# Kernel optimization log

Hardware: AMD Instinct MI355X
Metric: run time of the kernel (lower is better)

The kernel has to match this reference:

```python
import jax, jax.numpy as jnp
import numpy as np

NUM_USERS = 100000
NUM_ITEMS = 50000
N_NODES = NUM_USERS + NUM_ITEMS
LATENT_DIM = 64
N_LAYERS = 3
NNZ = 2400000
BATCH = 16384


def setup_inputs() -> dict:
    key = jax.random.key(0)
    k1, k2, k3, k4, k5, k6, k7 = jax.random.split(key, 7)
    user_emb = jax.random.normal(k1, (NUM_USERS, LATENT_DIM), dtype=jnp.float32) * 0.1
    item_emb = jax.random.normal(k2, (NUM_ITEMS, LATENT_DIM), dtype=jnp.float32) * 0.1
    edge_rows = jax.random.randint(k3, (NNZ,), 0, N_NODES, dtype=jnp.int32)
    edge_cols = jax.random.randint(k4, (NNZ,), 0, N_NODES, dtype=jnp.int32)
    # normalized-adjacency-like positive weights
    edge_vals = jax.random.uniform(k5, (NNZ,), dtype=jnp.float32) * 0.05
    user_input = jax.random.randint(k6, (BATCH,), 0, NUM_USERS, dtype=jnp.int64)
    item_input = jax.random.randint(k7, (BATCH,), 0, NUM_ITEMS, dtype=jnp.int64)
    return {
        "user_emb": user_emb,
        "item_emb": item_emb,
        "edge_rows": edge_rows,
        "edge_cols": edge_cols,
        "edge_vals": edge_vals,
        "user_input": user_input,
        "item_input": item_input,
    }


def _spmm(edge_rows, edge_cols, edge_vals, x):
    # sparse [N,N] @ dense [N,D] via gather + weighted segment-sum
    gathered = x[edge_cols] * edge_vals[:, None]  # [nnz, D]
    return jax.ops.segment_sum(gathered, edge_rows, num_segments=N_NODES)


def reference(user_emb, item_emb, edge_rows, edge_cols, edge_vals, user_input, item_input):
    all_emb = jnp.concatenate([user_emb, item_emb], axis=0)  # [N, D]
    acc = all_emb
    for _ in range(N_LAYERS):
        all_emb = _spmm(edge_rows, edge_cols, edge_vals, all_emb)
        acc = acc + all_emb
    light_out = acc / (N_LAYERS + 1)  # mean over stacked layer embeddings
    users_avg = light_out[:NUM_USERS]
    items_avg = light_out[NUM_USERS:]
    u = users_avg[user_input]  # [B, D]
    i = items_avg[item_input]  # [B, D]
    preds = jnp.sum(u * i, axis=1)  # [B]
    return preds
```

## Files before the change

kernel.cpp:

```cpp
#include <hip/hip_runtime.h>

#define NUM_USERS 100000
#define NUM_ITEMS 50000
#define N_NODES   150000
#define DIM       64
#define BATCH_N   16384
#define NPART     586

__global__ __launch_bounds__(256) void lg_init(const float4* __restrict__ user_emb,
                        const float4* __restrict__ item_emb,
                        float4* __restrict__ x,
                        float4* __restrict__ acc) {
    const long user4 = (long)NUM_USERS * DIM / 4;
    const long tot4  = (long)N_NODES  * DIM / 4;
    for (long i = blockIdx.x * (long)blockDim.x + threadIdx.x;
         i < tot4;
         i += (long)gridDim.x * blockDim.x) {
        float4 v = (i < user4) ? user_emb[i] : item_emb[i - user4];
        x[i]   = v;
        acc[i] = v;
    }
}

__global__ __launch_bounds__(256) void lg_hist(const int* __restrict__ rows,
                                               int* __restrict__ cnt, int nnz) {
    int e = blockIdx.x * blockDim.x + threadIdx.x;
    if (e < nnz) atomicAdd(&cnt[rows[e]], 1);
}

__global__ __launch_bounds__(256) void lg_scan1(const int* __restrict__ cnt,
                                                int* __restrict__ ptr,
                                                int* __restrict__ part) {
    __shared__ int s[256];
    int i = blockIdx.x * 256 + threadIdx.x;
    int v = (i < N_NODES) ? cnt[i] : 0;
    s[threadIdx.x] = v;
    __syncthreads();
    #pragma unroll
    for (int off = 1; off < 256; off <<= 1) {
        int t = (threadIdx.x >= off) ? s[threadIdx.x - off] : 0;
        __syncthreads();
        s[threadIdx.x] += t;
        __syncthreads();
    }
    if (i < N_NODES) ptr[i] = s[threadIdx.x] - v;
    if (threadIdx.x == 255) part[blockIdx.x] = s[255];
}

__global__ __launch_bounds__(64) void lg_scan2(int* __restrict__ part, int n) {
    int lane = threadIdx.x & 63;
    int run = 0;
    for (int base = 0; base < n; base += 64) {
        int i = base + lane;
        int v = (i < n) ? part[i] : 0;
        int orig = v;
        #pragma unroll
        for (int off = 1; off < 64; off <<= 1) {
            int t = __shfl_up(v, off, 64);
            if (lane >= off) v += t;
        }
        if (i < n) part[i] = run + v - orig;
        run += __shfl(v, 63, 64);
    }
}

__global__ __launch_bounds__(256) void lg_scan3(int* __restrict__ ptr,
                                                const int* __restrict__ part,
                                                int* __restrict__ cur) {
    int i = blockIdx.x * 256 + threadIdx.x;
    if (i < N_NODES) {
        int p = ptr[i] + part[blockIdx.x];
        ptr[i] = p;
        cur[i] = p;
    }
}

__global__ __launch_bounds__(256) void lg_scatter(const int* __restrict__ rows,
                           const int* __restrict__ cols,
                           const float* __restrict__ vals, int* __restrict__ cur,
                           int2* __restrict__ edges, int nnz) {
    int e = blockIdx.x * blockDim.x + threadIdx.x;
    if (e >= nnz) return;
    int r = rows[e];
    int pos = atomicAdd(&cur[r], 1);
    edges[pos] = make_int2(cols[e], __float_as_int(vals[e]));
}

template <bool WRITE_Y>
__global__ __launch_bounds__(256) void lg_spmm_csr(const int* __restrict__ ptr,
                            const int* __restrict__ cnt,
                            const int2* __restrict__ edges,
                            const float* __restrict__ x, float* __restrict__ y,
                            float* __restrict__ acc) {
    int r    = blockIdx.x * (blockDim.x >> 6) + (threadIdx.x >> 6);
    int lane = threadIdx.x & 63;
    if (r >= N_NODES) return;
    int start = __builtin_amdgcn_readfirstlane(ptr[r]);
    int len   = __builtin_amdgcn_readfirstlane(cnt[r]);
    const int2* __restrict__ ep = edges + start;
    float s0 = 0.0f, s1 = 0.0f;
    int j = 0;
    for (; j + 2 <= len; j += 2) {
        int2 e0 = ep[j];
        int2 e1 = ep[j + 1];
        s0 += __int_as_float(e0.y) * x[(long)e0.x * DIM + lane];
        s1 += __int_as_float(e1.y) * x[(long)e1.x * DIM + lane];
    }
    if (j < len) {
        int2 e0 = ep[j];
        s0 += __int_as_float(e0.y) * x[(long)e0.x * DIM + lane];
    }
    float sum = s0 + s1;
    long o = (long)r * DIM + lane;
    if (WRITE_Y) y[o] = sum;
    acc[o] += sum;
}

__global__ __launch_bounds__(256) void lg_dot(const float* __restrict__ acc,
                       const int*   __restrict__ uidx,
                       const int*   __restrict__ iidx,
                       float*       __restrict__ out,
                       int batch) {
    int b    = blockIdx.x * (blockDim.x >> 6) + (threadIdx.x >> 6);
    int lane = threadIdx.x & 63;
    if (b >= batch) return;
    long u = (long)uidx[b];
    long t = (long)NUM_USERS + iidx[b];
    float p = acc[u * DIM + lane] * acc[t * DIM + lane] * (1.0f / 16.0f);
    #pragma unroll
    for (int off = 32; off > 0; off >>= 1)
        p += __shfl_down(p, off, 64);
    if (lane == 0) out[b] = p;
}

extern "C" void kernel_launch(void* const* d_in, const int* in_sizes, int n_in,
                              void* d_out, int out_size, void* d_ws, size_t ws_size,
                              hipStream_t stream) {
    const float* user_emb  = (const float*)d_in[0];
    const float* item_emb  = (const float*)d_in[1];
    const int*   edge_rows = (const int*)  d_in[2];
    const int*   edge_cols = (const int*)  d_in[3];
    const float* edge_vals = (const float*)d_in[4];
    const int*   user_inp  = (const int*)  d_in[5];
    const int*   item_inp  = (const int*)  d_in[6];
    float*       out       = (float*)d_out;

    const int nnz = in_sizes[2];

    const size_t embBytes = (size_t)N_NODES * DIM * sizeof(float);
    const size_t nodeInts = (size_t)N_NODES * sizeof(int);
    const size_t need = 3 * embBytes + (size_t)nnz * 8 + 3 * nodeInts
                      + (size_t)NPART * sizeof(int);
    if (ws_size < need) return;

    char* ws = (char*)d_ws;
    float* x     = (float*)(ws);
    float* y     = (float*)(ws + embBytes);
    float* acc   = (float*)(ws + 2 * embBytes);
    int2*  edges = (int2*) (ws + 3 * embBytes);
    int*   cnt   = (int*)  (ws + 3 * embBytes + (size_t)nnz * 8);
    int*   ptr   = (int*)  (ws + 3 * embBytes + (size_t)nnz * 8 + nodeInts);
    int*   cur   = (int*)  (ws + 3 * embBytes + (size_t)nnz * 8 + 2 * nodeInts);
    int*   part  = (int*)  (ws + 3 * embBytes + (size_t)nnz * 8 + 3 * nodeInts);

    lg_init<<<2048, 256, 0, stream>>>((const float4*)user_emb,
                                      (const float4*)item_emb,
                                      (float4*)x, (float4*)acc);

    hipMemsetAsync(cnt, 0, nodeInts, stream);
    const int eb = (nnz + 255) / 256;
    lg_hist   <<<eb,    256, 0, stream>>>(edge_rows, cnt, nnz);
    lg_scan1  <<<NPART, 256, 0, stream>>>(cnt, ptr, part);
    lg_scan2  <<<1,      64, 0, stream>>>(part, NPART);
    lg_scan3  <<<NPART, 256, 0, stream>>>(ptr, part, cur);
    lg_scatter<<<eb,    256, 0, stream>>>(edge_rows, edge_cols, edge_vals,
                                          cur, edges, nnz);

    const int rowBlocks = (N_NODES + 3) / 4;
    lg_spmm_csr<true ><<<rowBlocks, 256, 0, stream>>>(ptr, cnt, edges, x, y, acc);
    lg_spmm_csr<true ><<<rowBlocks, 256, 0, stream>>>(ptr, cnt, edges, y, x, acc);
    lg_spmm_csr<false><<<rowBlocks, 256, 0, stream>>>(ptr, cnt, edges, x, y, acc);

    lg_dot<<<(BATCH_N + 3) / 4, 256, 0, stream>>>(acc, user_inp, item_inp,
                                                  out, BATCH_N);
}
```

Before: 703.9 us.

## Split edge scatter into row-range passes and unroll SpMM gather by four

The CSR scatter now runs as eight launches, each handling only edges whose destination row falls in one slice of the node range. This keeps the atomic cursor and edge-array write targets within a smaller footprint per pass, aiming for better cache locality of the random writes. The cost is re-reading the row array eight times. The SpMM inner loop is unrolled from two to four independent accumulators, and 64-bit index math is replaced by 32-bit shifts in SpMM and the dot kernel.

New measurement: 666.3 us. -5.3%, faster.

```diff
diff --git a/kernel.cpp b/kernel.cpp
--- a/kernel.cpp
+++ b/kernel.cpp
@@ -6,6 +6,8 @@
 #define DIM       64
 #define BATCH_N   16384
 #define NPART     586
+#define SC_PASSES 8
+#define SC_SLICE  18750
 
 __global__ __launch_bounds__(256) void lg_init(const float4* __restrict__ user_emb,
                         const float4* __restrict__ item_emb,
@@ -75,13 +77,14 @@
     }
 }
 
-__global__ __launch_bounds__(256) void lg_scatter(const int* __restrict__ rows,
+__global__ __launch_bounds__(256) void lg_scatter_pass(const int* __restrict__ rows,
                            const int* __restrict__ cols,
                            const float* __restrict__ vals, int* __restrict__ cur,
-                           int2* __restrict__ edges, int nnz) {
+                           int2* __restrict__ edges, int nnz, int lo, int hi) {
     int e = blockIdx.x * blockDim.x + threadIdx.x;
     if (e >= nnz) return;
     int r = rows[e];
+    if (r < lo || r >= hi) return;
     int pos = atomicAdd(&cur[r], 1);
     edges[pos] = make_int2(cols[e], __float_as_int(vals[e]));
 }
@@ -98,20 +101,24 @@
     int start = __builtin_amdgcn_readfirstlane(ptr[r]);
     int len   = __builtin_amdgcn_readfirstlane(cnt[r]);
     const int2* __restrict__ ep = edges + start;
-    float s0 = 0.0f, s1 = 0.0f;
+    float s0 = 0.0f, s1 = 0.0f, s2 = 0.0f, s3 = 0.0f;
     int j = 0;
-    for (; j + 2 <= len; j += 2) {
+    for (; j + 4 <= len; j += 4) {
         int2 e0 = ep[j];
         int2 e1 = ep[j + 1];
-        s0 += __int_as_float(e0.y) * x[(long)e0.x * DIM + lane];
-        s1 += __int_as_float(e1.y) * x[(long)e1.x * DIM + lane];
+        int2 e2 = ep[j + 2];
+        int2 e3 = ep[j + 3];
+        s0 += __int_as_float(e0.y) * x[(e0.x << 6) + lane];
+        s1 += __int_as_float(e1.y) * x[(e1.x << 6) + lane];
+        s2 += __int_as_float(e2.y) * x[(e2.x << 6) + lane];
+        s3 += __int_as_float(e3.y) * x[(e3.x << 6) + lane];
     }
-    if (j < len) {
+    for (; j < len; ++j) {
         int2 e0 = ep[j];
-        s0 += __int_as_float(e0.y) * x[(long)e0.x * DIM + lane];
+        s0 += __int_as_float(e0.y) * x[(e0.x << 6) + lane];
     }
-    float sum = s0 + s1;
-    long o = (long)r * DIM + lane;
+    float sum = (s0 + s1) + (s2 + s3);
+    int o = (r << 6) + lane;
     if (WRITE_Y) y[o] = sum;
     acc[o] += sum;
 }
@@ -124,9 +131,9 @@
     int b    = blockIdx.x * (blockDim.x >> 6) + (threadIdx.x >> 6);
     int lane = threadIdx.x & 63;
     if (b >= batch) return;
-    long u = (long)uidx[b];
-    long t = (long)NUM_USERS + iidx[b];
-    float p = acc[u * DIM + lane] * acc[t * DIM + lane] * (1.0f / 16.0f);
+    int u = uidx[b];
+    int t = NUM_USERS + iidx[b];
+    float p = acc[(u << 6) + lane] * acc[(t << 6) + lane] * (1.0f / 16.0f);
     #pragma unroll
     for (int off = 32; off > 0; off >>= 1)
         p += __shfl_down(p, off, 64);
@@ -169,12 +176,15 @@
 
     hipMemsetAsync(cnt, 0, nodeInts, stream);
     const int eb = (nnz + 255) / 256;
-    lg_hist   <<<eb,    256, 0, stream>>>(edge_rows, cnt, nnz);
-    lg_scan1  <<<NPART, 256, 0, stream>>>(cnt, ptr, part);
-    lg_scan2  <<<1,      64, 0, stream>>>(part, NPART);
-    lg_scan3  <<<NPART, 256, 0, stream>>>(ptr, part, cur);
-    lg_scatter<<<eb,    256, 0, stream>>>(edge_rows, edge_cols, edge_vals,
-                                          cur, edges, nnz);
+    lg_hist <<<eb,    256, 0, stream>>>(edge_rows, cnt, nnz);
+    lg_scan1<<<NPART, 256, 0, stream>>>(cnt, ptr, part);
+    lg_scan2<<<1,      64, 0, stream>>>(part, NPART);
+    lg_scan3<<<NPART, 256, 0, stream>>>(ptr, part, cur);
+    for (int p = 0; p < SC_PASSES; ++p) {
+        lg_scatter_pass<<<eb, 256, 0, stream>>>(edge_rows, edge_cols, edge_vals,
+                                                cur, edges, nnz,
+                                                p * SC_SLICE, (p + 1) * SC_SLICE);
+    }
 
     const int rowBlocks = (N_NODES + 3) / 4;
     lg_spmm_csr<true ><<<rowBlocks, 256, 0, stream>>>(ptr, cnt, edges, x, y, acc);
```
